# Optimization experiments

Hardware: AMD Instinct MI355X
Metric: run time of the kernel (lower is better)

## Reference

```python
import jax, jax.numpy as jnp
import numpy as np

IN_SIZE = 64
NUM_FEATURES = 32
NUM_HEADS = 8
EPS = 1e-5


def setup_inputs() -> dict:
    key = jax.random.key(0)
    ks = jax.random.split(key, 12)
    D, F, Hh = IN_SIZE, NUM_FEATURES, NUM_HEADS
    M = Hh * F  # MLP width = num_heads * num_features
    s = 0.05
    return {
        "x": jax.random.normal(ks[0], (2, D, 48, 48), dtype=jnp.float32),
        # stacked per-head projection weights, stored [in, out]
        "Wq": jax.random.normal(ks[1], (Hh, D, F), dtype=jnp.float32) * s,
        "bq": jax.random.normal(ks[2], (Hh, F), dtype=jnp.float32) * s,
        "Wk": jax.random.normal(ks[3], (Hh, D, F), dtype=jnp.float32) * s,
        "bk": jax.random.normal(ks[4], (Hh, F), dtype=jnp.float32) * s,
        "Wv": jax.random.normal(ks[5], (Hh, D, F), dtype=jnp.float32) * s,
        "bv": jax.random.normal(ks[6], (Hh, F), dtype=jnp.float32) * s,
        "W1": jax.random.normal(ks[7], (M, M), dtype=jnp.float32) * s,
        "b1": jax.random.normal(ks[8], (M,), dtype=jnp.float32) * s,
        "W2": jax.random.normal(ks[9], (M, M), dtype=jnp.float32) * s,
        "b2": jax.random.normal(ks[10], (M,), dtype=jnp.float32) * s,
        "gamma": jnp.ones((M,), dtype=jnp.float32),
        "beta": jnp.zeros((M,), dtype=jnp.float32),
    }


def _inorm_lastdim(y):
    # InstanceNorm1d applied to channels-last tensor: normalizes LAST dim,
    # biased variance, eps=1e-5, no affine.
    mu = jnp.mean(y, axis=-1, keepdims=True)
    var = jnp.mean(jnp.square(y - mu), axis=-1, keepdims=True)
    return (y - mu) / jnp.sqrt(var + EPS)


def reference(x, Wq, bq, Wk, bk, Wv, bv, W1, b1, W2, b2, gamma, beta):
    N, D, H, W = x.shape
    F = NUM_FEATURES
    L = H * W
    flat = jnp.transpose(x, (0, 2, 3, 1)).reshape(N, L, D)  # [N, L, D]

    def proj(Wm, bm):  # Wm [Hh, D, F], bm [Hh, F] -> [Hh, N, L, F]
        y = jnp.einsum('nld,hdf->hnlf', flat, Wm) + bm[:, None, None, :]
        return jax.nn.relu(_inorm_lastdim(y))

    Q = proj(Wq, bq)
    K = proj(Wk, bk)
    V = proj(Wv, bv)

    scores = jnp.einsum('hnlf,hnmf->hnlm', Q, K) / jnp.sqrt(jnp.float32(F))
    # original: F.softmax(scaled) on 3D [N,L,L] -> legacy dim=1 (first L axis)
    att = jax.nn.softmax(scores, axis=2)
    A = jnp.einsum('hnlm,hnmf->hnlf', att, V)  # [Hh, N, L, F]

    heads = jnp.transpose(A, (1, 2, 0, 3)).reshape(N, L, NUM_HEADS * F)
    m = jax.nn.relu(heads @ W1 + b1)
    m = jax.nn.relu(m @ W2 + b2)
    o = _inorm_lastdim(m + heads)
    o = gamma * o + beta  # [N, L, Hh*F]
    return jnp.transpose(o, (0, 2, 1)).reshape(N, NUM_HEADS * F, H, W)
```

## Files before the change

kernel.cpp:

```cpp
#include <hip/hip_runtime.h>
#include <hip/hip_bf16.h>
#include <stdint.h>

#define L_TOT 2304
#define D_IN  64
#define NF    32
#define NH    8
#define NB    2
#define MW    256
#define CHS   4
#define NSTRIP (L_TOT/32)
#define RT    32

constexpr float EPSV  = 1e-5f;
constexpr float SCALE = 0.17677669529663687f;
constexpr float SHIFT = 20.0f;

typedef __bf16  bf16x4  __attribute__((ext_vector_type(4)));
typedef __bf16  bf16x8  __attribute__((ext_vector_type(8)));
typedef float   f32x16  __attribute__((ext_vector_type(16)));

union U32x4BF { uint32_t u[4]; bf16x8 v; };

static __device__ __forceinline__ uint32_t pack_bf16(float a, float b) {
    union { __bf16 h[2]; uint32_t u; } r;
    r.h[0] = (__bf16)a;
    r.h[1] = (__bf16)b;
    return r.u;
}

__global__ void k_prep(const float* __restrict__ W1, const float* __restrict__ W2,
                       __hip_bfloat16* __restrict__ W1t, __hip_bfloat16* __restrict__ W2t)
{
    const float* src = blockIdx.z ? W2 : W1;
    __hip_bfloat16* dst = blockIdx.z ? W2t : W1t;
    __shared__ float t[32][33];
    const int bi = blockIdx.x * 32, bj = blockIdx.y * 32;
    #pragma unroll
    for (int k = 0; k < 4; ++k)
        t[threadIdx.y + 8*k][threadIdx.x] = src[(size_t)(bi + threadIdx.y + 8*k) * MW + bj + threadIdx.x];
    __syncthreads();
    #pragma unroll
    for (int k = 0; k < 4; ++k)
        dst[(size_t)(bj + threadIdx.y + 8*k) * MW + bi + threadIdx.x] =
            __float2bfloat16(t[threadIdx.x][threadIdx.y + 8*k]);
}

__global__ __launch_bounds__(1024) void k_proj(
    const float* __restrict__ x,
    const float* __restrict__ Wq, const float* __restrict__ bq,
    const float* __restrict__ Wk, const float* __restrict__ bk,
    const float* __restrict__ Wv, const float* __restrict__ bv,
    __hip_bfloat16* __restrict__ Qo, __hip_bfloat16* __restrict__ Ko,
    __hip_bfloat16* __restrict__ Vt)
{
    const int tile = blockIdx.x;
    const int n  = tile / (L_TOT / 16);
    const int l0 = (tile % (L_TOT / 16)) * 16;
    const int tid = threadIdx.x;
    const int rg = tid >> 8;
    const int h = (tid >> 5) & 7, f = tid & 31;
    const int r0 = rg * 4;

    __shared__ float xs[16][D_IN];
    __shared__ float Wl[D_IN * MW];

    for (int i = tid; i < 16 * D_IN; i += 1024) {
        int d = i >> 4, r = i & 15;
        xs[r][d] = x[n * D_IN * L_TOT + d * L_TOT + l0 + r];
    }

    const float* Ws[3] = {Wq, Wk, Wv};
    const float* bs[3] = {bq, bk, bv};
    const int hn = h * NB + n;
    const int strip = l0 >> 5;
    const int mbase = l0 & 31;

    #pragma unroll
    for (int mtx = 0; mtx < 3; ++mtx) {
        __syncthreads();
        {
            const float4* srcW = reinterpret_cast<const float4*>(Ws[mtx]);
            float4* dstW = reinterpret_cast<float4*>(Wl);
            #pragma unroll
            for (int i = 0; i < 4; ++i) dstW[tid + i * 1024] = srcW[tid + i * 1024];
        }
        __syncthreads();

        float acc[4] = {0.f, 0.f, 0.f, 0.f};
        const float* wp = Wl + h * (D_IN * NF) + f;
        for (int d = 0; d < D_IN; ++d) {
            float wv = wp[d * NF];
            #pragma unroll
            for (int rr = 0; rr < 4; ++rr) acc[rr] += xs[r0 + rr][d] * wv;
        }
        const float bias = bs[mtx][h * NF + f];
        __bf16 vtmp[4];
        #pragma unroll
        for (int rr = 0; rr < 4; ++rr) {
            const int r = r0 + rr;
            float v = acc[rr] + bias;
            float s = v, s2 = v * v;
            #pragma unroll
            for (int o = 16; o >= 1; o >>= 1) {
                s  += __shfl_xor(s,  o, 32);
                s2 += __shfl_xor(s2, o, 32);
            }
            float mu  = s  * (1.f / 32);
            float var = s2 * (1.f / 32) - mu * mu;
            float y = fmaxf((v - mu) * rsqrtf(var + EPSV), 0.f);
            if (mtx == 0) {
                Qo[((size_t)hn * L_TOT + l0 + r) * NF + f] = __float2bfloat16(y * SCALE);
            } else if (mtx == 1) {
                Ko[((size_t)hn * L_TOT + l0 + r) * NF + f] = __float2bfloat16(y);
            } else {
                vtmp[rr] = (__bf16)y;
            }
        }
        if (mtx == 2) {
            bf16x4* dst = reinterpret_cast<bf16x4*>(
                Vt + ((size_t)(hn * NSTRIP + strip) * 32 + f) * 32 + mbase + r0);
            bf16x4 vv = {vtmp[0], vtmp[1], vtmp[2], vtmp[3]};
            *dst = vv;
        }
    }
}

__global__ __launch_bounds__(256) void k_stats(
    const __hip_bfloat16* __restrict__ Qb, const __hip_bfloat16* __restrict__ Kb,
    float* __restrict__ zpart)
{
    const int w = threadIdx.x >> 6;
    const int strip = blockIdx.x * 4 + w;
    const int hn = blockIdx.y;
    const int chunk = blockIdx.z;
    const int lane = threadIdx.x & 63;
    const int c = lane & 31, hi = lane >> 5;

    const bf16x8* kp = reinterpret_cast<const bf16x8*>(
        Kb + ((size_t)hn * L_TOT + strip * 32 + c) * NF);
    const bf16x8 ka0 = kp[hi];
    const bf16x8 ka1 = kp[2 + hi];

    float Zr[16];
    #pragma unroll
    for (int r = 0; r < 16; ++r) Zr[r] = 0.f;

    for (int it = 0; it < (L_TOT / 32) / CHS; ++it) {
        const int l0 = (chunk * ((L_TOT / 32) / CHS) + it) * 32;
        const bf16x8* qp = reinterpret_cast<const bf16x8*>(
            Qb + ((size_t)hn * L_TOT + l0 + c) * NF);
        bf16x8 qb0 = qp[hi];
        bf16x8 qb1 = qp[2 + hi];
        f32x16 s16 = {};
        s16 = __builtin_amdgcn_mfma_f32_32x32x16_bf16(ka0, qb0, s16, 0, 0, 0);
        s16 = __builtin_amdgcn_mfma_f32_32x32x16_bf16(ka1, qb1, s16, 0, 0, 0);
        #pragma unroll
        for (int r = 0; r < 16; ++r) Zr[r] += __expf(s16[r] - SHIFT);
    }
    #pragma unroll
    for (int r = 0; r < 16; ++r) {
        #pragma unroll
        for (int o = 16; o >= 1; o >>= 1) Zr[r] += __shfl_xor(Zr[r], o, 64);
    }
    if (c == 0) {
        float4* zp = reinterpret_cast<float4*>(
            zpart + ((size_t)chunk * 16 + hn) * L_TOT + strip * 32 + hi * 16);
        zp[0] = make_float4(Zr[0], Zr[1], Zr[2], Zr[3]);
        zp[1] = make_float4(Zr[4], Zr[5], Zr[6], Zr[7]);
        zp[2] = make_float4(Zr[8], Zr[9], Zr[10], Zr[11]);
        zp[3] = make_float4(Zr[12], Zr[13], Zr[14], Zr[15]);
    }
}

__global__ __launch_bounds__(256) void k_finish(
    const float* __restrict__ zpart, float* __restrict__ lse_p)
{
    const int idx = blockIdx.x * 256 + threadIdx.x;
    float Z = 0.f;
    #pragma unroll
    for (int cc = 0; cc < CHS; ++cc) Z += zpart[(size_t)cc * 16 * L_TOT + idx];
    lse_p[idx] = SHIFT + logf(Z);
}

__global__ __launch_bounds__(256) void k_apply(
    const __hip_bfloat16* __restrict__ Qb, const __hip_bfloat16* __restrict__ Kb,
    const __hip_bfloat16* __restrict__ Vt, const float* __restrict__ lse_p,
    float* __restrict__ partA, int CH)
{
    const int w = threadIdx.x >> 6;
    const int ltile = blockIdx.x * 4 + w;
    const int l0 = ltile * 32;
    const int hn = blockIdx.y;
    const int chunk = blockIdx.z;
    const int lane = threadIdx.x & 63;
    const int c = lane & 31, hi = lane >> 5;

    const bf16x8* qp = reinterpret_cast<const bf16x8*>(
        Qb + ((size_t)hn * L_TOT + l0 + c) * NF);
    const bf16x8 qb0 = qp[hi];
    const bf16x8 qb1 = qp[2 + hi];

    f32x16 acc = {};
    const int nsteps = NSTRIP / CH;

    for (int it = 0; it < nsteps; ++it) {
        const int st = chunk * nsteps + it;
        const bf16x8* kp = reinterpret_cast<const bf16x8*>(
            Kb + ((size_t)hn * L_TOT + st * 32 + c) * NF);
        f32x16 s16 = {};
        s16 = __builtin_amdgcn_mfma_f32_32x32x16_bf16(kp[hi], qb0, s16, 0, 0, 0);
        s16 = __builtin_amdgcn_mfma_f32_32x32x16_bf16(kp[2 + hi], qb1, s16, 0, 0, 0);

        const float4* lp = reinterpret_cast<const float4*>(
            lse_p + (size_t)hn * L_TOT + st * 32 + hi * 16);
        float lv[16];
        #pragma unroll
        for (int q = 0; q < 4; ++q) {
            float4 t = lp[q];
            lv[4 * q + 0] = t.x; lv[4 * q + 1] = t.y;
            lv[4 * q + 2] = t.z; lv[4 * q + 3] = t.w;
        }
        float p[16];
        #pragma unroll
        for (int r = 0; r < 16; ++r) p[r] = __expf(s16[r] - lv[r]);

        uint32_t wp[8];
        #pragma unroll
        for (int q = 0; q < 8; ++q) wp[q] = pack_bf16(p[2 * q], p[2 * q + 1]);

        uint32_t sendA = hi ? wp[0] : wp[2];
        uint32_t sendB = hi ? wp[1] : wp[3];
        uint32_t rA = (uint32_t)__shfl_xor((int)sendA, 32, 64);
        uint32_t rB = (uint32_t)__shfl_xor((int)sendB, 32, 64);
        U32x4BF fragP0;
        fragP0.u[0] = hi ? rA    : wp[0];
        fragP0.u[1] = hi ? rB    : wp[1];
        fragP0.u[2] = hi ? wp[2] : rA;
        fragP0.u[3] = hi ? wp[3] : rB;
        uint32_t sendC = hi ? wp[4] : wp[6];
        uint32_t sendD = hi ? wp[5] : wp[7];
        uint32_t rC = (uint32_t)__shfl_xor((int)sendC, 32, 64);
        uint32_t rD = (uint32_t)__shfl_xor((int)sendD, 32, 64);
        U32x4BF fragP1;
        fragP1.u[0] = hi ? rC    : wp[4];
        fragP1.u[1] = hi ? rD    : wp[5];
        fragP1.u[2] = hi ? wp[6] : rC;
        fragP1.u[3] = hi ? wp[7] : rD;

        const bf16x8* vp = reinterpret_cast<const bf16x8*>(
            Vt + ((size_t)(hn * NSTRIP + st) * 32 + c) * 32);
        acc = __builtin_amdgcn_mfma_f32_32x32x16_bf16(fragP0.v, vp[hi], acc, 0, 0, 0);
        acc = __builtin_amdgcn_mfma_f32_32x32x16_bf16(fragP1.v, vp[2 + hi], acc, 0, 0, 0);
    }

    const int n = hn & 1, h = hn >> 1;
    float* outp = partA + (size_t)chunk * (NB * L_TOT * MW)
                + ((size_t)(n * L_TOT + l0)) * MW + h * NF + c;
    #pragma unroll
    for (int r = 0; r < 16; ++r) {
        int row = (r & 3) + 8 * (r >> 2) + 4 * hi;
        outp[(size_t)row * MW] = acc[r];
    }
}

__global__ __launch_bounds__(512) void k_mlp(
    const float* __restrict__ partA,
    const __hip_bfloat16* __restrict__ W1t, const float* __restrict__ b1,
    const __hip_bfloat16* __restrict__ W2t, const float* __restrict__ b2,
    const float* __restrict__ gamma, const float* __restrict__ beta,
    float* __restrict__ out, int CH)
{
    const int blk = blockIdx.x;
    const int n  = blk / (L_TOT / RT);
    const int l0 = (blk % (L_TOT / RT)) * RT;
    const int tid = threadIdx.x;
    const int w = tid >> 6, lane = tid & 63;
    const int c = lane & 31, hi = lane >> 5;
    const int n0 = w * 32;

    __shared__ __align__(16) char smem[67584];
    float (*hsf)[MW] = reinterpret_cast<float (*)[MW]>(smem);
    __hip_bfloat16 (*hA)[264]  = reinterpret_cast<__hip_bfloat16 (*)[264]>(smem + 32768);
    __hip_bfloat16 (*msb)[264] = reinterpret_cast<__hip_bfloat16 (*)[264]>(smem + 49664);
    float (*ys)[MW] = reinterpret_cast<float (*)[MW]>(smem + 32768);
    float (*rs)[4]  = reinterpret_cast<float (*)[4]>(smem + 66560);
    float (*rs2)[4] = reinterpret_cast<float (*)[4]>(smem + 67072);

    for (int idx = tid; idx < RT * MW; idx += 512) {
        int r = idx >> 8, i = idx & 255;
        float v = 0.f;
        for (int k = 0; k < CH; ++k)
            v += partA[(size_t)k * (NB * L_TOT * MW) + ((size_t)n * L_TOT + l0 + r) * MW + i];
        hsf[r][i] = v;
        hA[r][i] = __float2bfloat16(v);
    }
    __syncthreads();

    const float bb1 = b1[n0 + c];
    bf16x8 B1[16];
    #pragma unroll
    for (int k0 = 0; k0 < 16; ++k0)
        B1[k0] = *reinterpret_cast<const bf16x8*>(W1t + (size_t)(n0 + c) * MW + k0 * 16 + hi * 8);
    f32x16 acc = {};
    #pragma unroll
    for (int k0 = 0; k0 < 16; ++k0) {
        bf16x8 a = *reinterpret_cast<const bf16x8*>(&hA[c][k0 * 16 + hi * 8]);
        acc = __builtin_amdgcn_mfma_f32_32x32x16_bf16(a, B1[k0], acc, 0, 0, 0);
    }
    #pragma unroll
    for (int r = 0; r < 16; ++r) {
        int row = (r & 3) + 8 * (r >> 2) + 4 * hi;
        msb[row][n0 + c] = __float2bfloat16(fmaxf(acc[r] + bb1, 0.f));
    }
    __syncthreads();

    const float bb2 = b2[n0 + c];
    bf16x8 B2[16];
    #pragma unroll
    for (int k0 = 0; k0 < 16; ++k0)
        B2[k0] = *reinterpret_cast<const bf16x8*>(W2t + (size_t)(n0 + c) * MW + k0 * 16 + hi * 8);
    f32x16 acc2 = {};
    #pragma unroll
    for (int k0 = 0; k0 < 16; ++k0) {
        bf16x8 a = *reinterpret_cast<const bf16x8*>(&msb[c][k0 * 16 + hi * 8]);
        acc2 = __builtin_amdgcn_mfma_f32_32x32x16_bf16(a, B2[k0], acc2, 0, 0, 0);
    }
    float yv[16];
    #pragma unroll
    for (int r = 0; r < 16; ++r) {
        int row = (r & 3) + 8 * (r >> 2) + 4 * hi;
        yv[r] = fmaxf(acc2[r] + bb2, 0.f) + hsf[row][n0 + c];
    }
    __syncthreads();
    #pragma unroll
    for (int r = 0; r < 16; ++r) {
        int row = (r & 3) + 8 * (r >> 2) + 4 * hi;
        ys[row][n0 + c] = yv[r];
    }
    __syncthreads();

    const int col = tid & 255;
    const int half = tid >> 8;
    const int wid = (tid >> 6) & 3;
    float vv[16];
    #pragma unroll
    for (int r = 0; r < 16; ++r) {
        float v = ys[half * 16 + r][col];
        vv[r] = v;
        float s = v, s2 = v * v;
        #pragma unroll
        for (int o = 32; o >= 1; o >>= 1) { s += __shfl_xor(s, o, 64); s2 += __shfl_xor(s2, o, 64); }
        if (lane == 0) { rs[half * 16 + r][wid] = s; rs2[half * 16 + r][wid] = s2; }
    }
    __syncthreads();
    const float g = gamma[col], be = beta[col];
    float ov[16];
    #pragma unroll
    for (int r = 0; r < 16; ++r) {
        int row = half * 16 + r;
        float s  = rs[row][0]  + rs[row][1]  + rs[row][2]  + rs[row][3];
        float s2 = rs2[row][0] + rs2[row][1] + rs2[row][2] + rs2[row][3];
        float mu  = s  * (1.f / MW);
        float var = s2 * (1.f / MW) - mu * mu;
        ov[r] = g * ((vv[r] - mu) * rsqrtf(var + EPSV)) + be;
    }
    float* ob = out + ((size_t)n * MW + col) * L_TOT + l0 + half * 16;
    #pragma unroll
    for (int q = 0; q < 4; ++q)
        reinterpret_cast<float4*>(ob)[q] =
            make_float4(ov[4 * q], ov[4 * q + 1], ov[4 * q + 2], ov[4 * q + 3]);
}

extern "C" void kernel_launch(void* const* d_in, const int* in_sizes, int n_in,
                              void* d_out, int out_size, void* d_ws, size_t ws_size,
                              hipStream_t stream) {
    const float* x  = (const float*)d_in[0];
    const float* Wq = (const float*)d_in[1];
    const float* bq = (const float*)d_in[2];
    const float* Wk = (const float*)d_in[3];
    const float* bk = (const float*)d_in[4];
    const float* Wv = (const float*)d_in[5];
    const float* bv = (const float*)d_in[6];
    const float* W1 = (const float*)d_in[7];
    const float* b1 = (const float*)d_in[8];
    const float* W2 = (const float*)d_in[9];
    const float* b2 = (const float*)d_in[10];
    const float* gm = (const float*)d_in[11];
    const float* bt = (const float*)d_in[12];
    float* out = (float*)d_out;

    const size_t QKVE = (size_t)16 * L_TOT * NF;
    const size_t BF_BYTES = 3 * QKVE * sizeof(__hip_bfloat16);
    const size_t ZN = (size_t)CHS * 16 * L_TOT;
    const size_t LN = (size_t)16 * L_TOT;
    const size_t WTE = (size_t)MW * MW;
    const size_t HEADS = (size_t)NB * L_TOT * MW;

    __hip_bfloat16* Qb = (__hip_bfloat16*)d_ws;
    __hip_bfloat16* Kb = Qb + QKVE;
    __hip_bfloat16* Vt = Kb + QKVE;
    float* zpart = (float*)((char*)d_ws + BF_BYTES);
    float* lse_p = zpart + ZN;
    __hip_bfloat16* W1t = (__hip_bfloat16*)(lse_p + LN);
    __hip_bfloat16* W2t = W1t + WTE;
    float* partA = (float*)(W2t + WTE);

    const size_t fixed = BF_BYTES + (ZN + LN) * sizeof(float) + 2 * WTE * sizeof(__hip_bfloat16);
    int CH = 1;
    for (int cc = 4; cc >= 2; cc >>= 1) {
        if (fixed + (size_t)cc * HEADS * sizeof(float) <= ws_size) { CH = cc; break; }
    }

    k_prep<<<dim3(8, 8, 2), dim3(32, 8), 0, stream>>>(W1, W2, W1t, W2t);
    k_proj<<<dim3(NB * (L_TOT / 16)), dim3(1024), 0, stream>>>(
        x, Wq, bq, Wk, bk, Wv, bv, Qb, Kb, Vt);
    k_stats<<<dim3(NSTRIP / 4, 16, CHS), dim3(256), 0, stream>>>(Qb, Kb, zpart);
    k_finish<<<dim3(16 * L_TOT / 256), dim3(256), 0, stream>>>(zpart, lse_p);
    k_apply<<<dim3(NSTRIP / 4, 16, CH), dim3(256), 0, stream>>>(
        Qb, Kb, Vt, lse_p, partA, CH);
    k_mlp<<<dim3(NB * (L_TOT / RT)), dim3(512), 0, stream>>>(
        partA, W1t, b1, W2t, b2, gm, bt, out, CH);
}
```

Measured before the change: 137.5 us.

## Move QKV projection to bf16 MFMA and drop split-K chunking in apply

Adds a prep kernel that converts x and the QKV weights to bf16 in transposed layouts. The QKV projection is rewritten so each wavefront computes a 32x32 tile with MFMA, and the instance norm is done in registers instead of through per-thread fp32 loops over shared memory. Separately, k_apply no longer splits the key dimension into chunks. It writes one partA buffer, so k_mlp no longer has to sum partials. This reduces memory traffic and fp32 ALU work, but k_apply now exposes less parallelism and there is one extra launch.

```diff
diff --git a/kernel.cpp b/kernel.cpp
--- a/kernel.cpp
+++ b/kernel.cpp
@@ -16,7 +16,6 @@
 constexpr float SCALE = 0.17677669529663687f;
 constexpr float SHIFT = 20.0f;
 
-typedef __bf16  bf16x4  __attribute__((ext_vector_type(4)));
 typedef __bf16  bf16x8  __attribute__((ext_vector_type(8)));
 typedef float   f32x16  __attribute__((ext_vector_type(16)));
 
@@ -46,82 +45,126 @@
             __float2bfloat16(t[threadIdx.x][threadIdx.y + 8*k]);
 }
 
-__global__ __launch_bounds__(1024) void k_proj(
+__global__ __launch_bounds__(256) void k_prep2(
     const float* __restrict__ x,
-    const float* __restrict__ Wq, const float* __restrict__ bq,
-    const float* __restrict__ Wk, const float* __restrict__ bk,
-    const float* __restrict__ Wv, const float* __restrict__ bv,
+    const float* __restrict__ Wq, const float* __restrict__ Wk, const float* __restrict__ Wv,
+    __hip_bfloat16* __restrict__ xb, __hip_bfloat16* __restrict__ Wqkvt)
+{
+    const int job = blockIdx.x;
+    const int tx = threadIdx.x & 31, ty = threadIdx.x >> 5;
+    const float* src;
+    size_t sstride;
+    __hip_bfloat16* dst;
+    if (job < 24) {
+        int mtx = job >> 3, h = job & 7;
+        const float* Wm = mtx == 0 ? Wq : (mtx == 1 ? Wk : Wv);
+        src = Wm + (size_t)h * D_IN * NF;
+        sstride = NF;
+        dst = Wqkvt + (size_t)job * NF * D_IN;
+    } else {
+        int i = job - 24;
+        int n = i / NSTRIP, lt = i % NSTRIP;
+        src = x + (size_t)n * D_IN * L_TOT + lt * 32;
+        sstride = L_TOT;
+        dst = xb + ((size_t)n * L_TOT + lt * 32) * D_IN;
+    }
+    __shared__ float t[64][33];
+    #pragma unroll
+    for (int k = 0; k < 8; ++k)
+        t[ty + 8 * k][tx] = src[(size_t)(ty + 8 * k) * sstride + tx];
+    __syncthreads();
+    #pragma unroll
+    for (int k = 0; k < 4; ++k) {
+        int col = ty + 8 * k;
+        #pragma unroll
+        for (int j = 0; j < 2; ++j)
+            dst[(size_t)col * D_IN + tx + 32 * j] = __float2bfloat16(t[tx + 32 * j][col]);
+    }
+}
+
+__global__ __launch_bounds__(256) void k_proj(
+    const __hip_bfloat16* __restrict__ xb, const __hip_bfloat16* __restrict__ Wqkvt,
+    const float* __restrict__ bq, const float* __restrict__ bk, const float* __restrict__ bv,
     __hip_bfloat16* __restrict__ Qo, __hip_bfloat16* __restrict__ Ko,
     __hip_bfloat16* __restrict__ Vt)
 {
-    const int tile = blockIdx.x;
-    const int n  = tile / (L_TOT / 16);
-    const int l0 = (tile % (L_TOT / 16)) * 16;
-    const int tid = threadIdx.x;
-    const int rg = tid >> 8;
-    const int h = (tid >> 5) & 7, f = tid & 31;
-    const int r0 = rg * 4;
-
-    __shared__ float xs[16][D_IN];
-    __shared__ float Wl[D_IN * MW];
-
-    for (int i = tid; i < 16 * D_IN; i += 1024) {
-        int d = i >> 4, r = i & 15;
-        xs[r][d] = x[n * D_IN * L_TOT + d * L_TOT + l0 + r];
-    }
-
-    const float* Ws[3] = {Wq, Wk, Wv};
+    const int ltile = blockIdx.x;
+    const int n = blockIdx.y;
+    const int h = blockIdx.z * 4 + (threadIdx.x >> 6);
+    const int l0 = ltile * 32;
+    const int lane = threadIdx.x & 63;
+    const int c = lane & 31, hi = lane >> 5;
+    const int hn = h * NB + n;
+
+    const bf16x8* xp = reinterpret_cast<const bf16x8*>(
+        xb + ((size_t)n * L_TOT + l0 + c) * D_IN);
+    bf16x8 xf[4];
+    #pragma unroll
+    for (int t = 0; t < 4; ++t) xf[t] = xp[2 * t + hi];
+
     const float* bs[3] = {bq, bk, bv};
-    const int hn = h * NB + n;
-    const int strip = l0 >> 5;
-    const int mbase = l0 & 31;
 
     #pragma unroll
     for (int mtx = 0; mtx < 3; ++mtx) {
-        __syncthreads();
-        {
-            const float4* srcW = reinterpret_cast<const float4*>(Ws[mtx]);
-            float4* dstW = reinterpret_cast<float4*>(Wl);
+        const bf16x8* wp = reinterpret_cast<const bf16x8*>(
+            Wqkvt + ((size_t)(mtx * NH + h) * NF + c) * D_IN);
+        f32x16 acc = {};
+        #pragma unroll
+        for (int t = 0; t < 4; ++t)
+            acc = __builtin_amdgcn_mfma_f32_32x32x16_bf16(wp[2 * t + hi], xf[t], acc, 0, 0, 0);
+
+        float bb[16];
+        #pragma unroll
+        for (int g = 0; g < 4; ++g) {
+            float4 t4 = *reinterpret_cast<const float4*>(&bs[mtx][h * NF + 8 * g + 4 * hi]);
+            bb[4 * g + 0] = t4.x; bb[4 * g + 1] = t4.y;
+            bb[4 * g + 2] = t4.z; bb[4 * g + 3] = t4.w;
+        }
+
+        float v[16], s = 0.f, s2 = 0.f;
+        #pragma unroll
+        for (int r = 0; r < 16; ++r) {
+            v[r] = acc[r] + bb[r];
+            s += v[r]; s2 += v[r] * v[r];
+        }
+        s  += __shfl_xor(s, 32, 64);
+        s2 += __shfl_xor(s2, 32, 64);
+        float mu = s * (1.f / 32);
+        float rstd = rsqrtf(s2 * (1.f / 32) - mu * mu + EPSV);
+        float y[16];
+        #pragma unroll
+        for (int r = 0; r < 16; ++r) y[r] = fmaxf((v[r] - mu) * rstd, 0.f);
+
+        if (mtx == 2) {
             #pragma unroll
-            for (int i = 0; i < 4; ++i) dstW[tid + i * 1024] = srcW[tid + i * 1024];
-        }
-        __syncthreads();
-
-        float acc[4] = {0.f, 0.f, 0.f, 0.f};
-        const float* wp = Wl + h * (D_IN * NF) + f;
-        for (int d = 0; d < D_IN; ++d) {
-            float wv = wp[d * NF];
+            for (int r = 0; r < 16; ++r) {
+                int f = (r & 3) + 8 * (r >> 2) + 4 * hi;
+                Vt[((size_t)(hn * NSTRIP + ltile) * NF + f) * 32 + c] = __float2bfloat16(y[r]);
+            }
+        } else {
+            if (mtx == 0) {
+                #pragma unroll
+                for (int r = 0; r < 16; ++r) y[r] *= SCALE;
+            }
+            uint32_t pk[8];
             #pragma unroll
-            for (int rr = 0; rr < 4; ++rr) acc[rr] += xs[r0 + rr][d] * wv;
-        }
-        const float bias = bs[mtx][h * NF + f];
-        __bf16 vtmp[4];
-        #pragma unroll
-        for (int rr = 0; rr < 4; ++rr) {
-            const int r = r0 + rr;
-            float v = acc[rr] + bias;
-            float s = v, s2 = v * v;
+            for (int q = 0; q < 8; ++q) pk[q] = pack_bf16(y[2 * q], y[2 * q + 1]);
+            uint32_t rr[4];
             #pragma unroll
-            for (int o = 16; o >= 1; o >>= 1) {
-                s  += __shfl_xor(s,  o, 32);
-                s2 += __shfl_xor(s2, o, 32);
+            for (int j = 0; j < 4; ++j)
+                rr[j] = (uint32_t)__shfl_xor((int)(hi ? pk[j] : pk[4 + j]), 32, 64);
+            uint32_t row[8];
+            if (hi == 0) {
+                row[0] = pk[0]; row[1] = pk[1]; row[2] = rr[0]; row[3] = rr[1];
+                row[4] = pk[2]; row[5] = pk[3]; row[6] = rr[2]; row[7] = rr[3];
+            } else {
+                row[0] = rr[0]; row[1] = rr[1]; row[2] = pk[4]; row[3] = pk[5];
+                row[4] = rr[2]; row[5] = rr[3]; row[6] = pk[6]; row[7] = pk[7];
             }
-            float mu  = s  * (1.f / 32);
-            float var = s2 * (1.f / 32) - mu * mu;
-            float y = fmaxf((v - mu) * rsqrtf(var + EPSV), 0.f);
-            if (mtx == 0) {
-                Qo[((size_t)hn * L_TOT + l0 + r) * NF + f] = __float2bfloat16(y * SCALE);
-            } else if (mtx == 1) {
-                Ko[((size_t)hn * L_TOT + l0 + r) * NF + f] = __float2bfloat16(y);
-            } else {
-                vtmp[rr] = (__bf16)y;
-            }
-        }
-        if (mtx == 2) {
-            bf16x4* dst = reinterpret_cast<bf16x4*>(
-                Vt + ((size_t)(hn * NSTRIP + strip) * 32 + f) * 32 + mbase + r0);
-            bf16x4 vv = {vtmp[0], vtmp[1], vtmp[2], vtmp[3]};
-            *dst = vv;
+            __hip_bfloat16* dst = (mtx == 0 ? Qo : Ko)
+                + ((size_t)hn * L_TOT + l0 + c) * NF + hi * 16;
+            reinterpret_cast<uint4*>(dst)[0] = make_uint4(row[0], row[1], row[2], row[3]);
+            reinterpret_cast<uint4*>(dst)[1] = make_uint4(row[4], row[5], row[6], row[7]);
         }
     }
 }
@@ -186,13 +229,12 @@
 __global__ __launch_bounds__(256) void k_apply(
     const __hip_bfloat16* __restrict__ Qb, const __hip_bfloat16* __restrict__ Kb,
     const __hip_bfloat16* __restrict__ Vt, const float* __restrict__ lse_p,
-    float* __restrict__ partA, int CH)
+    float* __restrict__ partA)
 {
     const int w = threadIdx.x >> 6;
     const int ltile = blockIdx.x * 4 + w;
     const int l0 = ltile * 32;
     const int hn = blockIdx.y;
-    const int chunk = blockIdx.z;
     const int lane = threadIdx.x & 63;
     const int c = lane & 31, hi = lane >> 5;
 
@@ -202,10 +244,8 @@
     const bf16x8 qb1 = qp[2 + hi];
 
     f32x16 acc = {};
-    const int nsteps = NSTRIP / CH;
-
-    for (int it = 0; it < nsteps; ++it) {
-        const int st = chunk * nsteps + it;
+
+    for (int st = 0; st < NSTRIP; ++st) {
         const bf16x8* kp = reinterpret_cast<const bf16x8*>(
             Kb + ((size_t)hn * L_TOT + st * 32 + c) * NF);
         f32x16 s16 = {};
@@ -249,14 +289,13 @@
         fragP1.u[3] = hi ? wp[7] : rD;
 
         const bf16x8* vp = reinterpret_cast<const bf16x8*>(
-            Vt + ((size_t)(hn * NSTRIP + st) * 32 + c) * 32);
+            Vt + ((size_t)(hn * NSTRIP + st) * NF + c) * 32);
         acc = __builtin_amdgcn_mfma_f32_32x32x16_bf16(fragP0.v, vp[hi], acc, 0, 0, 0);
         acc = __builtin_amdgcn_mfma_f32_32x32x16_bf16(fragP1.v, vp[2 + hi], acc, 0, 0, 0);
     }
 
     const int n = hn & 1, h = hn >> 1;
-    float* outp = partA + (size_t)chunk * (NB * L_TOT * MW)
-                + ((size_t)(n * L_TOT + l0)) * MW + h * NF + c;
+    float* outp = partA + ((size_t)(n * L_TOT + l0)) * MW + h * NF + c;
     #pragma unroll
     for (int r = 0; r < 16; ++r) {
         int row = (r & 3) + 8 * (r >> 2) + 4 * hi;
@@ -269,7 +308,7 @@
     const __hip_bfloat16* __restrict__ W1t, const float* __restrict__ b1,
     const __hip_bfloat16* __restrict__ W2t, const float* __restrict__ b2,
     const float* __restrict__ gamma, const float* __restrict__ beta,
-    float* __restrict__ out, int CH)
+    float* __restrict__ out)
 {
     const int blk = blockIdx.x;
     const int n  = blk / (L_TOT / RT);
@@ -289,9 +328,7 @@
 
     for (int idx = tid; idx < RT * MW; idx += 512) {
         int r = idx >> 8, i = idx & 255;
-        float v = 0.f;
-        for (int k = 0; k < CH; ++k)
-            v += partA[(size_t)k * (NB * L_TOT * MW) + ((size_t)n * L_TOT + l0 + r) * MW + i];
+        float v = partA[((size_t)n * L_TOT + l0 + r) * MW + i];
         hsf[r][i] = v;
         hA[r][i] = __float2bfloat16(v);
     }
@@ -391,34 +428,31 @@
     float* out = (float*)d_out;
 
     const size_t QKVE = (size_t)16 * L_TOT * NF;
-    const size_t BF_BYTES = 3 * QKVE * sizeof(__hip_bfloat16);
+    const size_t XBE  = (size_t)NB * L_TOT * D_IN;
+    const size_t WQE  = (size_t)3 * NH * NF * D_IN;
+    const size_t WTE  = (size_t)MW * MW;
     const size_t ZN = (size_t)CHS * 16 * L_TOT;
     const size_t LN = (size_t)16 * L_TOT;
-    const size_t WTE = (size_t)MW * MW;
-    const size_t HEADS = (size_t)NB * L_TOT * MW;
 
     __hip_bfloat16* Qb = (__hip_bfloat16*)d_ws;
     __hip_bfloat16* Kb = Qb + QKVE;
     __hip_bfloat16* Vt = Kb + QKVE;
-    float* zpart = (float*)((char*)d_ws + BF_BYTES);
+    __hip_bfloat16* xb = Vt + QKVE;
+    __hip_bfloat16* Wqkvt = xb + XBE;
+    __hip_bfloat16* W1t = Wqkvt + WQE;
+    __hip_bfloat16* W2t = W1t + WTE;
+    float* zpart = (float*)(W2t + WTE);
     float* lse_p = zpart + ZN;
-    __hip_bfloat16* W1t = (__hip_bfloat16*)(lse_p + LN);
-    __hip_bfloat16* W2t = W1t + WTE;
-    float* partA = (float*)(W2t + WTE);
-
-    const size_t fixed = BF_BYTES + (ZN + LN) * sizeof(float) + 2 * WTE * sizeof(__hip_bfloat16);
-    int CH = 1;
-    for (int cc = 4; cc >= 2; cc >>= 1) {
-        if (fixed + (size_t)cc * HEADS * sizeof(float) <= ws_size) { CH = cc; break; }
-    }
+    float* partA = lse_p + LN;
 
     k_prep<<<dim3(8, 8, 2), dim3(32, 8), 0, stream>>>(W1, W2, W1t, W2t);
-    k_proj<<<dim3(NB * (L_TOT / 16)), dim3(1024), 0, stream>>>(
-        x, Wq, bq, Wk, bk, Wv, bv, Qb, Kb, Vt);
+    k_prep2<<<dim3(24 + NB * NSTRIP), dim3(256), 0, stream>>>(x, Wq, Wk, Wv, xb, Wqkvt);
+    k_proj<<<dim3(NSTRIP, NB, 2), dim3(256), 0, stream>>>(
+        xb, Wqkvt, bq, bk, bv, Qb, Kb, Vt);
     k_stats<<<dim3(NSTRIP / 4, 16, CHS), dim3(256), 0, stream>>>(Qb, Kb, zpart);
     k_finish<<<dim3(16 * L_TOT / 256), dim3(256), 0, stream>>>(zpart, lse_p);
-    k_apply<<<dim3(NSTRIP / 4, 16, CH), dim3(256), 0, stream>>>(
-        Qb, Kb, Vt, lse_p, partA, CH);
+    k_apply<<<dim3(NSTRIP / 4, 16), dim3(256), 0, stream>>>(
+        Qb, Kb, Vt, lse_p, partA);
     k_mlp<<<dim3(NB * (L_TOT / RT)), dim3(512), 0, stream>>>(
-        partA, W1t, b1, W2t, b2, gm, bt, out, CH);
-}
+        partA, W1t, b1, W2t, b2, gm, bt, out);
+}
```

After: 143.6 us. 1.04x slower.
